# Kernel optimization log

Measured on AMD Instinct MI355X. Metric: run time of the kernel, lower is better.

## Reference

```python
import jax, jax.numpy as jnp
import numpy as np

EPS = float(jnp.finfo(jnp.float32).eps)  # torch F.rms_norm default eps


def _rope(x, cos, sin):
    # x: [B,T,H,D]; cos/sin: [1,T,1,D//2]
    d = x.shape[-1] // 2
    x1, x2 = x[..., :d], x[..., d:]
    return jnp.concatenate([x1 * cos + x2 * sin, -x1 * sin + x2 * cos], axis=-1)


def _rmsnorm(x):
    ms = jnp.mean(jnp.square(x), axis=-1, keepdims=True)
    return x * jax.lax.rsqrt(ms + EPS)


def setup_inputs() -> dict:
    key = jax.random.key(0)
    ks = jax.random.split(key, 7)
    B, T, C, H, D = 2, 2048, 2048, 16, 128
    x = jax.random.normal(ks[0], (B, T, C), dtype=jnp.float32)
    # RoPE tables (use actual rotary angles for realism)
    pos = jnp.arange(T, dtype=jnp.float32)[:, None]
    inv_freq = 1.0 / (10000.0 ** (jnp.arange(0, D // 2, dtype=jnp.float32) / (D // 2)))
    ang = pos * inv_freq[None, :]  # [T, D/2]
    cos = jnp.cos(ang)[None, :, None, :]
    sin = jnp.sin(ang)[None, :, None, :]
    w_scale = 0.02
    wq = jax.random.normal(ks[1], (C, C), dtype=jnp.float32) * w_scale
    wk = jax.random.normal(ks[2], (C, C), dtype=jnp.float32) * w_scale
    wv = jax.random.normal(ks[3], (C, C), dtype=jnp.float32) * w_scale
    wproj = jax.random.normal(ks[4], (C, C), dtype=jnp.float32) * w_scale
    return {"x": x, "cos": cos, "sin": sin, "wq": wq, "wk": wk, "wv": wv, "wproj": wproj}


def reference(x, cos, sin, wq, wk, wv, wproj):
    B, T, C = x.shape
    H, D = 16, C // 16
    q = (x @ wq.T).reshape(B, T, H, D)
    k = (x @ wk.T).reshape(B, T, H, D)
    v = (x @ wv.T).reshape(B, T, H, D)
    q = _rmsnorm(_rope(q, cos, sin))
    k = _rmsnorm(_rope(k, cos, sin))
    scale = 1.0 / jnp.sqrt(jnp.asarray(D, dtype=x.dtype))
    # causal attention: logits [B,H,T,T]
    logits = jnp.einsum('bqhd,bkhd->bhqk', q, k) * scale
    causal = jnp.tril(jnp.ones((T, T), dtype=bool))
    logits = jnp.where(causal[None, None], logits, jnp.finfo(x.dtype).min)
    attn = jax.nn.softmax(logits, axis=-1)
    y = jnp.einsum('bhqk,bkhd->bqhd', attn, v).reshape(B, T, C)
    return y @ wproj.T
```

## Files before the change

### kernel.cpp

```cpp
#include <hip/hip_runtime.h>
#include <hip/hip_bf16.h>
#include <cstdint>
#include <cstddef>

typedef unsigned short u16;
typedef unsigned int u32;
typedef __attribute__((ext_vector_type(4))) float f32x4;
typedef __attribute__((ext_vector_type(8))) __bf16 bf16x8;

#define EPS_F 1.1920928955078125e-07f
#define INV_SQRT_D 0.08838834764831845f

__device__ __forceinline__ u16 f2bf(float f) {
  union { float f; u32 u; } v; v.f = f;
  u32 r = v.u + 0x7fffu + ((v.u >> 16) & 1u);
  return (u16)(r >> 16);
}

__device__ __forceinline__ ushort4 pack_bf4(float a, float b, float c, float d) {
  ushort4 o; o.x = f2bf(a); o.y = f2bf(b); o.z = f2bf(c); o.w = f2bf(d); return o;
}

__device__ __forceinline__ void gload_lds16(const void* g, void* l) {
  __builtin_amdgcn_global_load_lds((const __attribute__((address_space(1))) u32*)g,
                                   (__attribute__((address_space(3))) u32*)l, 16, 0, 0);
}

__global__ __launch_bounds__(256) void k_cast_bf16(const float* __restrict__ src,
                                                   u16* __restrict__ dst, int n) {
  int i = (blockIdx.x * 256 + threadIdx.x) * 4;
  if (i + 3 < n) {
    float4 v = *(const float4*)(src + i);
    *(ushort4*)(dst + i) = pack_bf4(v.x, v.y, v.z, v.w);
  }
}

__global__ __launch_bounds__(256) void k_gemm_bt(const u16* __restrict__ A,
                                                 const u16* __restrict__ Bw,
                                                 float* __restrict__ C,
                                                 int M, int N, int K) {
  __shared__ __align__(16) u16 As[128 * 32];
  __shared__ __align__(16) u16 Bs[128 * 32];
  const int tid = threadIdx.x;
  const int lane = tid & 63;
  const int wid = tid >> 6;
  const int wm = wid >> 1, wn = wid & 1;
  const int l15 = lane & 15, l4 = lane >> 4;

  f32x4 acc[4][4];
#pragma unroll
  for (int i = 0; i < 4; ++i)
#pragma unroll
    for (int j = 0; j < 4; ++j) acc[i][j] = {0.f, 0.f, 0.f, 0.f};

  const u16* Ab = A + (size_t)blockIdx.x * 128 * K;
  const u16* Bb = Bw + (size_t)blockIdx.y * 128 * K;
  const int lrow = lane >> 2;
  const int scol = ((lane & 3) ^ ((lane >> 3) & 3)) * 8;
  const int rswz = (l15 >> 1) & 3;

  for (int k0 = 0; k0 < K; k0 += 32) {
    __syncthreads();
#pragma unroll
    for (int p = 0; p < 2; ++p) {
      const int chunk = wid * 2 + p;
      const int row = chunk * 16 + lrow;
      gload_lds16(Ab + (size_t)row * K + k0 + scol, &As[chunk * 512]);
      gload_lds16(Bb + (size_t)row * K + k0 + scol, &Bs[chunk * 512]);
    }
    __syncthreads();
    bf16x8 af[4], bfv[4];
#pragma unroll
    for (int i = 0; i < 4; ++i) {
      const int cb = (l4 ^ rswz) * 8;
      af[i]  = *(const bf16x8*)&As[(wm * 64 + i * 16 + l15) * 32 + cb];
      bfv[i] = *(const bf16x8*)&Bs[(wn * 64 + i * 16 + l15) * 32 + cb];
    }
#pragma unroll
    for (int i = 0; i < 4; ++i)
#pragma unroll
      for (int j = 0; j < 4; ++j)
        acc[i][j] = __builtin_amdgcn_mfma_f32_16x16x32_bf16(af[i], bfv[j], acc[i][j], 0, 0, 0);
  }

  const int r0 = blockIdx.x * 128 + wm * 64 + l4 * 4;
  const int c0 = blockIdx.y * 128 + wn * 64 + l15;
#pragma unroll
  for (int i = 0; i < 4; ++i)
#pragma unroll
    for (int j = 0; j < 4; ++j) {
      float* Cp = C + (size_t)(r0 + i * 16) * N + c0 + j * 16;
#pragma unroll
      for (int r = 0; r < 4; ++r) Cp[(size_t)r * N] = acc[i][j][r];
    }
}

__global__ __launch_bounds__(256) void k_rope_rms(const float* __restrict__ qkv,
                                                  const float* __restrict__ cosp,
                                                  const float* __restrict__ sinp,
                                                  u16* __restrict__ qb, u16* __restrict__ kb,
                                                  u16* __restrict__ vb) {
  const int T = 2048;
  const int m = blockIdx.x;
  const int b = m >> 11;
  const int t = m & 2047;
  const int tid = threadIdx.x;
  const int h = tid >> 4;
  const int d0 = (tid & 15) * 4;
  const size_t ro = (size_t)m * 6144 + h * 128;

  float4 q1 = *(const float4*)(qkv + ro + d0);
  float4 q2 = *(const float4*)(qkv + ro + d0 + 64);
  float4 k1 = *(const float4*)(qkv + ro + 2048 + d0);
  float4 k2 = *(const float4*)(qkv + ro + 2048 + d0 + 64);
  float4 v1 = *(const float4*)(qkv + ro + 4096 + d0);
  float4 v2 = *(const float4*)(qkv + ro + 4096 + d0 + 64);
  float4 cs = *(const float4*)(cosp + (size_t)t * 64 + d0);
  float4 sn = *(const float4*)(sinp + (size_t)t * 64 + d0);

  float sq = q1.x*q1.x + q1.y*q1.y + q1.z*q1.z + q1.w*q1.w
           + q2.x*q2.x + q2.y*q2.y + q2.z*q2.z + q2.w*q2.w;
  float sk = k1.x*k1.x + k1.y*k1.y + k1.z*k1.z + k1.w*k1.w
           + k2.x*k2.x + k2.y*k2.y + k2.z*k2.z + k2.w*k2.w;
#pragma unroll
  for (int o = 1; o < 16; o <<= 1) {
    sq += __shfl_xor(sq, o, 64);
    sk += __shfl_xor(sk, o, 64);
  }
  const float rq = rsqrtf(sq * (1.f / 128.f) + EPS_F) * INV_SQRT_D;
  const float rk = rsqrtf(sk * (1.f / 128.f) + EPS_F);

  const size_t ob = ((size_t)(b * 16 + h) * T + t) * 128 + d0;
  *(ushort4*)(qb + ob) = pack_bf4((q1.x*cs.x + q2.x*sn.x) * rq, (q1.y*cs.y + q2.y*sn.y) * rq,
                                  (q1.z*cs.z + q2.z*sn.z) * rq, (q1.w*cs.w + q2.w*sn.w) * rq);
  *(ushort4*)(qb + ob + 64) = pack_bf4((q2.x*cs.x - q1.x*sn.x) * rq, (q2.y*cs.y - q1.y*sn.y) * rq,
                                       (q2.z*cs.z - q1.z*sn.z) * rq, (q2.w*cs.w - q1.w*sn.w) * rq);
  *(ushort4*)(kb + ob) = pack_bf4((k1.x*cs.x + k2.x*sn.x) * rk, (k1.y*cs.y + k2.y*sn.y) * rk,
                                  (k1.z*cs.z + k2.z*sn.z) * rk, (k1.w*cs.w + k2.w*sn.w) * rk);
  *(ushort4*)(kb + ob + 64) = pack_bf4((k2.x*cs.x - k1.x*sn.x) * rk, (k2.y*cs.y - k1.y*sn.y) * rk,
                                       (k2.z*cs.z - k1.z*sn.z) * rk, (k2.w*cs.w - k1.w*sn.w) * rk);
  *(ushort4*)(vb + ob) = pack_bf4(v1.x, v1.y, v1.z, v1.w);
  *(ushort4*)(vb + ob + 64) = pack_bf4(v2.x, v2.y, v2.z, v2.w);
}

__global__ __launch_bounds__(256) void k_transpose_v(const u16* __restrict__ vb,
                                                     u16* __restrict__ vt) {
  const int T = 2048;
  __shared__ u16 tile[32][33];
  const int bh = blockIdx.z;
  const int t0 = blockIdx.x * 32;
  const int d0 = blockIdx.y * 32;
  const int tx = threadIdx.x & 31;
  const int ty = threadIdx.x >> 5;
  const size_t base = (size_t)bh * T * 128;
#pragma unroll
  for (int i = 0; i < 4; ++i)
    tile[ty + i * 8][tx] = vb[base + (size_t)(t0 + ty + i * 8) * 128 + d0 + tx];
  __syncthreads();
#pragma unroll
  for (int i = 0; i < 4; ++i)
    vt[base + (size_t)(d0 + ty + i * 8) * T + t0 + tx] = tile[tx][ty + i * 8];
}

__global__ __launch_bounds__(256) void k_attn(const u16* __restrict__ qb,
                                              const u16* __restrict__ kb,
                                              const u16* __restrict__ vt,
                                              u16* __restrict__ y) {
  const int T = 2048;
  __shared__ __align__(16) u16 Ks[64 * 128];
  __shared__ __align__(16) u16 Vs[128 * 64];
  __shared__ __align__(16) u16 Ps[64 * 72];

  const int tid = threadIdx.x;
  const int lane = tid & 63;
  const int wid = tid >> 6;
  const int bh = blockIdx.y;
  const int q0 = blockIdx.x * 64;
  const int b = bh >> 4, h = bh & 15;
  const size_t hb = (size_t)bh * T * 128;
  const int l15 = lane & 15, l4 = lane >> 4;

  bf16x8 qf[4];
  {
    const int qrow = q0 + wid * 16 + l15;
#pragma unroll
    for (int ki = 0; ki < 4; ++ki)
      qf[ki] = *(const bf16x8*)(qb + hb + (size_t)qrow * 128 + ki * 32 + l4 * 8);
  }

  float mrow[4], lsum[4];
  f32x4 oacc[8];
#pragma unroll
  for (int r = 0; r < 4; ++r) { mrow[r] = -INFINITY; lsum[r] = 0.f; }
#pragma unroll
  for (int d = 0; d < 8; ++d) oacc[d] = {0.f, 0.f, 0.f, 0.f};

  const int niter = blockIdx.x + 1;
  for (int it = 0; it < niter; ++it) {
    const int kv0 = it * 64;
    __syncthreads();
#pragma unroll
    for (int p = 0; p < 4; ++p) {
      const int chunk = wid * 4 + p;
      {
        const int row = chunk * 4 + l4;
        const int scb = l15 ^ (row & 7);
        gload_lds16(kb + hb + (size_t)(kv0 + row) * 128 + scb * 8, &Ks[chunk * 512]);
      }
      {
        const int row = chunk * 8 + (lane >> 3);
        const int scb = (lane & 7) ^ (row & 7);
        gload_lds16(vt + hb + (size_t)row * T + kv0 + scb * 8, &Vs[chunk * 512]);
      }
    }
    __syncthreads();

    f32x4 s[4];
#pragma unroll
    for (int ni = 0; ni < 4; ++ni) {
      s[ni] = {0.f, 0.f, 0.f, 0.f};
      const int r = ni * 16 + l15;
#pragma unroll
      for (int ki = 0; ki < 4; ++ki) {
        const int cb = (ki * 4 + l4) ^ (r & 7);
        bf16x8 kf = *(const bf16x8*)&Ks[r * 128 + cb * 8];
        s[ni] = __builtin_amdgcn_mfma_f32_16x16x32_bf16(qf[ki], kf, s[ni], 0, 0, 0);
      }
    }

    if (kv0 == q0) {
      const int grow = q0 + wid * 16 + l4 * 4;
      const int gcol = kv0 + l15;
#pragma unroll
      for (int ni = 0; ni < 4; ++ni)
#pragma unroll
        for (int r = 0; r < 4; ++r)
          if (gcol + ni * 16 > grow + r) s[ni][r] = -INFINITY;
    }

    float pv[4][4];
    float alpha[4];
#pragma unroll
    for (int r = 0; r < 4; ++r) {
      float mx = fmaxf(fmaxf(s[0][r], s[1][r]), fmaxf(s[2][r], s[3][r]));
#pragma unroll
      for (int o = 1; o < 16; o <<= 1) mx = fmaxf(mx, __shfl_xor(mx, o, 64));
      const float mnew = fmaxf(mrow[r], mx);
      alpha[r] = __expf(mrow[r] - mnew);
      mrow[r] = mnew;
      float ps = 0.f;
#pragma unroll
      for (int ni = 0; ni < 4; ++ni) {
        const float p = __expf(s[ni][r] - mnew);
        pv[ni][r] = p;
        ps += p;
      }
#pragma unroll
      for (int o = 1; o < 16; o <<= 1) ps += __shfl_xor(ps, o, 64);
      lsum[r] = lsum[r] * alpha[r] + ps;
    }
#pragma unroll
    for (int d = 0; d < 8; ++d) {
      f32x4 tv = oacc[d];
      tv[0] *= alpha[0]; tv[1] *= alpha[1]; tv[2] *= alpha[2]; tv[3] *= alpha[3];
      oacc[d] = tv;
    }
#pragma unroll
    for (int ni = 0; ni < 4; ++ni)
#pragma unroll
      for (int r = 0; r < 4; ++r)
        Ps[(wid * 16 + l4 * 4 + r) * 72 + ni * 16 + l15] = f2bf(pv[ni][r]);
    __syncthreads();

#pragma unroll
    for (int k2 = 0; k2 < 2; ++k2) {
      bf16x8 pa = *(const bf16x8*)&Ps[(wid * 16 + l15) * 72 + k2 * 32 + l4 * 8];
#pragma unroll
      for (int dt = 0; dt < 8; ++dt) {
        const int r = dt * 16 + l15;
        const int cb = (k2 * 4 + l4) ^ (r & 7);
        bf16x8 vf = *(const bf16x8*)&Vs[r * 64 + cb * 8];
        oacc[dt] = __builtin_amdgcn_mfma_f32_16x16x32_bf16(pa, vf, oacc[dt], 0, 0, 0);
      }
    }
  }

#pragma unroll
  for (int r = 0; r < 4; ++r) {
    const float inv = 1.f / lsum[r];
    const size_t yo = ((size_t)(b * T) + q0 + wid * 16 + l4 * 4 + r) * 2048 + h * 128;
#pragma unroll
    for (int dt = 0; dt < 8; ++dt)
      y[yo + dt * 16 + l15] = f2bf(oacc[dt][r] * inv);
  }
}

extern "C" void kernel_launch(void* const* d_in, const int* in_sizes, int n_in,
                              void* d_out, int out_size, void* d_ws, size_t ws_size,
                              hipStream_t stream) {
  const float* x     = (const float*)d_in[0];
  const float* cosp  = (const float*)d_in[1];
  const float* sinp  = (const float*)d_in[2];
  const float* wq    = (const float*)d_in[3];
  const float* wk    = (const float*)d_in[4];
  const float* wv    = (const float*)d_in[5];
  const float* wproj = (const float*)d_in[6];
  float* out = (float*)d_out;

  const int T = 2048, C = 2048;
  const int M = 2 * T;
  const int N1 = 3 * C;

  char* ws = (char*)d_ws;
  size_t off = 0;
  auto take = [&](size_t bytes) -> char* {
    char* p = ws + off;
    off += (bytes + 255) & ~(size_t)255;
    return p;
  };
  u16* xb    = (u16*)take((size_t)M * C * 2);
  u16* wqkvb = (u16*)take((size_t)N1 * C * 2);
  u16* wpb   = (u16*)take((size_t)C * C * 2);
  float* qkv = (float*)take((size_t)M * N1 * 4);
  u16* qb    = (u16*)take((size_t)M * C * 2);
  u16* kb    = (u16*)take((size_t)M * C * 2);
  u16* vb    = (u16*)take((size_t)M * C * 2);
  u16* vt    = (u16*)take((size_t)M * C * 2);
  u16* yb    = (u16*)take((size_t)M * C * 2);
  (void)ws_size; (void)in_sizes; (void)n_in; (void)out_size;

  const int nx = M * C;
  const int nw = C * C;
  k_cast_bf16<<<nx / 1024, 256, 0, stream>>>(x, xb, nx);
  k_cast_bf16<<<nw / 1024, 256, 0, stream>>>(wq, wqkvb, nw);
  k_cast_bf16<<<nw / 1024, 256, 0, stream>>>(wk, wqkvb + (size_t)C * C, nw);
  k_cast_bf16<<<nw / 1024, 256, 0, stream>>>(wv, wqkvb + (size_t)2 * C * C, nw);
  k_cast_bf16<<<nw / 1024, 256, 0, stream>>>(wproj, wpb, nw);

  k_gemm_bt<<<dim3(M / 128, N1 / 128), 256, 0, stream>>>(xb, wqkvb, qkv, M, N1, C);
  k_rope_rms<<<M, 256, 0, stream>>>(qkv, cosp, sinp, qb, kb, vb);
  k_transpose_v<<<dim3(T / 32, 128 / 32, 32), 256, 0, stream>>>(vb, vt);
  k_attn<<<dim3(T / 64, 32), 256, 0, stream>>>(qb, kb, vt, yb);
  k_gemm_bt<<<dim3(M / 128, C / 128), 256, 0, stream>>>(yb, wpb, out, M, C, C);
}
```

Measured before the change: 547.3 us.

## Double-buffer K/V tiles, pair causal query tiles, use exp2 softmax

The attention kernel now double-buffers the K and V tiles in LDS. The next tile's global-to-LDS load is issued before computing on the current one, with a single barrier per iteration instead of two. Each block processes two query tiles (qt and 31-qt), so every block gets the same amount of causal work; the grid is halved to match. The softmax scale is folded together with log2(e) into the q normalization so exp2f replaces __expf. In exchange, LDS use doubles, which may lower occupancy, and there are fewer blocks in flight.

```diff
diff --git a/kernel.cpp b/kernel.cpp
--- a/kernel.cpp
+++ b/kernel.cpp
@@ -10,6 +10,7 @@
 
 #define EPS_F 1.1920928955078125e-07f
 #define INV_SQRT_D 0.08838834764831845f
+#define LOG2E 1.4426950408889634f
 
 __device__ __forceinline__ u16 f2bf(float f) {
   union { float f; u32 u; } v; v.f = f;
@@ -127,7 +128,7 @@
     sq += __shfl_xor(sq, o, 64);
     sk += __shfl_xor(sk, o, 64);
   }
-  const float rq = rsqrtf(sq * (1.f / 128.f) + EPS_F) * INV_SQRT_D;
+  const float rq = rsqrtf(sq * (1.f / 128.f) + EPS_F) * (INV_SQRT_D * LOG2E);
   const float rk = rsqrtf(sk * (1.f / 128.f) + EPS_F);
 
   const size_t ob = ((size_t)(b * 16 + h) * T + t) * 128 + d0;
@@ -167,131 +168,148 @@
                                               const u16* __restrict__ vt,
                                               u16* __restrict__ y) {
   const int T = 2048;
-  __shared__ __align__(16) u16 Ks[64 * 128];
-  __shared__ __align__(16) u16 Vs[128 * 64];
+  __shared__ __align__(16) u16 Ks[2][64 * 128];
+  __shared__ __align__(16) u16 Vs[2][128 * 64];
   __shared__ __align__(16) u16 Ps[64 * 72];
 
   const int tid = threadIdx.x;
   const int lane = tid & 63;
   const int wid = tid >> 6;
   const int bh = blockIdx.y;
-  const int q0 = blockIdx.x * 64;
   const int b = bh >> 4, h = bh & 15;
   const size_t hb = (size_t)bh * T * 128;
   const int l15 = lane & 15, l4 = lane >> 4;
 
-  bf16x8 qf[4];
-  {
-    const int qrow = q0 + wid * 16 + l15;
-#pragma unroll
-    for (int ki = 0; ki < 4; ++ki)
-      qf[ki] = *(const bf16x8*)(qb + hb + (size_t)qrow * 128 + ki * 32 + l4 * 8);
-  }
-
-  float mrow[4], lsum[4];
-  f32x4 oacc[8];
-#pragma unroll
-  for (int r = 0; r < 4; ++r) { mrow[r] = -INFINITY; lsum[r] = 0.f; }
-#pragma unroll
-  for (int d = 0; d < 8; ++d) oacc[d] = {0.f, 0.f, 0.f, 0.f};
-
-  const int niter = blockIdx.x + 1;
-  for (int it = 0; it < niter; ++it) {
-    const int kv0 = it * 64;
-    __syncthreads();
+  auto stage = [&](int it, int buf) {
 #pragma unroll
     for (int p = 0; p < 4; ++p) {
       const int chunk = wid * 4 + p;
       {
         const int row = chunk * 4 + l4;
         const int scb = l15 ^ (row & 7);
-        gload_lds16(kb + hb + (size_t)(kv0 + row) * 128 + scb * 8, &Ks[chunk * 512]);
+        gload_lds16(kb + hb + (size_t)(it * 64 + row) * 128 + scb * 8, &Ks[buf][chunk * 512]);
       }
       {
         const int row = chunk * 8 + (lane >> 3);
         const int scb = (lane & 7) ^ (row & 7);
-        gload_lds16(vt + hb + (size_t)row * T + kv0 + scb * 8, &Vs[chunk * 512]);
-      }
-    }
-    __syncthreads();
-
-    f32x4 s[4];
-#pragma unroll
-    for (int ni = 0; ni < 4; ++ni) {
-      s[ni] = {0.f, 0.f, 0.f, 0.f};
-      const int r = ni * 16 + l15;
-#pragma unroll
-      for (int ki = 0; ki < 4; ++ki) {
-        const int cb = (ki * 4 + l4) ^ (r & 7);
-        bf16x8 kf = *(const bf16x8*)&Ks[r * 128 + cb * 8];
-        s[ni] = __builtin_amdgcn_mfma_f32_16x16x32_bf16(qf[ki], kf, s[ni], 0, 0, 0);
-      }
-    }
-
-    if (kv0 == q0) {
-      const int grow = q0 + wid * 16 + l4 * 4;
-      const int gcol = kv0 + l15;
+        gload_lds16(vt + hb + (size_t)row * T + it * 64 + scb * 8, &Vs[buf][chunk * 512]);
+      }
+    }
+  };
+
+#pragma unroll 1
+  for (int ph = 0; ph < 2; ++ph) {
+    const int qt = (ph == 0) ? (int)blockIdx.x : 31 - (int)blockIdx.x;
+    const int q0 = qt * 64;
+    const int niter = qt + 1;
+
+    bf16x8 qf[4];
+    {
+      const int qrow = q0 + wid * 16 + l15;
+#pragma unroll
+      for (int ki = 0; ki < 4; ++ki)
+        qf[ki] = *(const bf16x8*)(qb + hb + (size_t)qrow * 128 + ki * 32 + l4 * 8);
+    }
+
+    float mrow[4], lsum[4];
+    f32x4 oacc[8];
+#pragma unroll
+    for (int r = 0; r < 4; ++r) { mrow[r] = -INFINITY; lsum[r] = 0.f; }
+#pragma unroll
+    for (int d = 0; d < 8; ++d) oacc[d] = {0.f, 0.f, 0.f, 0.f};
+
+    stage(0, 0);
+    asm volatile("s_waitcnt vmcnt(0)" ::: "memory");
+    __builtin_amdgcn_s_barrier();
+    __builtin_amdgcn_sched_barrier(0);
+
+    int cur = 0;
+#pragma unroll 1
+    for (int it = 0; it < niter; ++it) {
+      if (it + 1 < niter) stage(it + 1, cur ^ 1);
+
+      f32x4 s[4];
+#pragma unroll
+      for (int ni = 0; ni < 4; ++ni) {
+        s[ni] = {0.f, 0.f, 0.f, 0.f};
+        const int r = ni * 16 + l15;
+#pragma unroll
+        for (int ki = 0; ki < 4; ++ki) {
+          const int cb = (ki * 4 + l4) ^ (r & 7);
+          bf16x8 kf = *(const bf16x8*)&Ks[cur][r * 128 + cb * 8];
+          s[ni] = __builtin_amdgcn_mfma_f32_16x16x32_bf16(qf[ki], kf, s[ni], 0, 0, 0);
+        }
+      }
+
+      if (it == niter - 1) {
+        const int grow = q0 + wid * 16 + l4 * 4;
+        const int gcol = it * 64 + l15;
+#pragma unroll
+        for (int ni = 0; ni < 4; ++ni)
+#pragma unroll
+          for (int r = 0; r < 4; ++r)
+            if (gcol + ni * 16 > grow + r) s[ni][r] = -INFINITY;
+      }
+
+      float pv[4][4];
+      float alpha[4];
+#pragma unroll
+      for (int r = 0; r < 4; ++r) {
+        float mx = fmaxf(fmaxf(s[0][r], s[1][r]), fmaxf(s[2][r], s[3][r]));
+#pragma unroll
+        for (int o = 1; o < 16; o <<= 1) mx = fmaxf(mx, __shfl_xor(mx, o, 64));
+        const float mnew = fmaxf(mrow[r], mx);
+        alpha[r] = exp2f(mrow[r] - mnew);
+        mrow[r] = mnew;
+        float ps = 0.f;
+#pragma unroll
+        for (int ni = 0; ni < 4; ++ni) {
+          const float p = exp2f(s[ni][r] - mnew);
+          pv[ni][r] = p;
+          ps += p;
+        }
+#pragma unroll
+        for (int o = 1; o < 16; o <<= 1) ps += __shfl_xor(ps, o, 64);
+        lsum[r] = lsum[r] * alpha[r] + ps;
+      }
+#pragma unroll
+      for (int d = 0; d < 8; ++d) {
+        f32x4 tv = oacc[d];
+        tv[0] *= alpha[0]; tv[1] *= alpha[1]; tv[2] *= alpha[2]; tv[3] *= alpha[3];
+        oacc[d] = tv;
+      }
 #pragma unroll
       for (int ni = 0; ni < 4; ++ni)
 #pragma unroll
         for (int r = 0; r < 4; ++r)
-          if (gcol + ni * 16 > grow + r) s[ni][r] = -INFINITY;
-    }
-
-    float pv[4][4];
-    float alpha[4];
+          Ps[(wid * 16 + l4 * 4 + r) * 72 + ni * 16 + l15] = f2bf(pv[ni][r]);
+
+#pragma unroll
+      for (int k2 = 0; k2 < 2; ++k2) {
+        bf16x8 pa = *(const bf16x8*)&Ps[(wid * 16 + l15) * 72 + k2 * 32 + l4 * 8];
+#pragma unroll
+        for (int dt = 0; dt < 8; ++dt) {
+          const int r = dt * 16 + l15;
+          const int cb = (k2 * 4 + l4) ^ (r & 7);
+          bf16x8 vf = *(const bf16x8*)&Vs[cur][r * 64 + cb * 8];
+          oacc[dt] = __builtin_amdgcn_mfma_f32_16x16x32_bf16(pa, vf, oacc[dt], 0, 0, 0);
+        }
+      }
+
+      asm volatile("s_waitcnt vmcnt(0)" ::: "memory");
+      __builtin_amdgcn_s_barrier();
+      __builtin_amdgcn_sched_barrier(0);
+      cur ^= 1;
+    }
+
 #pragma unroll
     for (int r = 0; r < 4; ++r) {
-      float mx = fmaxf(fmaxf(s[0][r], s[1][r]), fmaxf(s[2][r], s[3][r]));
-#pragma unroll
-      for (int o = 1; o < 16; o <<= 1) mx = fmaxf(mx, __shfl_xor(mx, o, 64));
-      const float mnew = fmaxf(mrow[r], mx);
-      alpha[r] = __expf(mrow[r] - mnew);
-      mrow[r] = mnew;
-      float ps = 0.f;
-#pragma unroll
-      for (int ni = 0; ni < 4; ++ni) {
-        const float p = __expf(s[ni][r] - mnew);
-        pv[ni][r] = p;
-        ps += p;
-      }
-#pragma unroll
-      for (int o = 1; o < 16; o <<= 1) ps += __shfl_xor(ps, o, 64);
-      lsum[r] = lsum[r] * alpha[r] + ps;
-    }
-#pragma unroll
-    for (int d = 0; d < 8; ++d) {
-      f32x4 tv = oacc[d];
-      tv[0] *= alpha[0]; tv[1] *= alpha[1]; tv[2] *= alpha[2]; tv[3] *= alpha[3];
-      oacc[d] = tv;
-    }
-#pragma unroll
-    for (int ni = 0; ni < 4; ++ni)
-#pragma unroll
-      for (int r = 0; r < 4; ++r)
-        Ps[(wid * 16 + l4 * 4 + r) * 72 + ni * 16 + l15] = f2bf(pv[ni][r]);
-    __syncthreads();
-
-#pragma unroll
-    for (int k2 = 0; k2 < 2; ++k2) {
-      bf16x8 pa = *(const bf16x8*)&Ps[(wid * 16 + l15) * 72 + k2 * 32 + l4 * 8];
-#pragma unroll
-      for (int dt = 0; dt < 8; ++dt) {
-        const int r = dt * 16 + l15;
-        const int cb = (k2 * 4 + l4) ^ (r & 7);
-        bf16x8 vf = *(const bf16x8*)&Vs[r * 64 + cb * 8];
-        oacc[dt] = __builtin_amdgcn_mfma_f32_16x16x32_bf16(pa, vf, oacc[dt], 0, 0, 0);
-      }
-    }
-  }
-
-#pragma unroll
-  for (int r = 0; r < 4; ++r) {
-    const float inv = 1.f / lsum[r];
-    const size_t yo = ((size_t)(b * T) + q0 + wid * 16 + l4 * 4 + r) * 2048 + h * 128;
-#pragma unroll
-    for (int dt = 0; dt < 8; ++dt)
-      y[yo + dt * 16 + l15] = f2bf(oacc[dt][r] * inv);
+      const float inv = 1.f / lsum[r];
+      const size_t yo = ((size_t)(b * T) + q0 + wid * 16 + l4 * 4 + r) * 2048 + h * 128;
+#pragma unroll
+      for (int dt = 0; dt < 8; ++dt)
+        y[yo + dt * 16 + l15] = f2bf(oacc[dt][r] * inv);
+    }
   }
 }
 
@@ -340,6 +358,6 @@
   k_gemm_bt<<<dim3(M / 128, N1 / 128), 256, 0, stream>>>(xb, wqkvb, qkv, M, N1, C);
   k_rope_rms<<<M, 256, 0, stream>>>(qkv, cosp, sinp, qb, kb, vb);
   k_transpose_v<<<dim3(T / 32, 128 / 32, 32), 256, 0, stream>>>(vb, vt);
-  k_attn<<<dim3(T / 64, 32), 256, 0, stream>>>(qb, kb, vt, yb);
+  k_attn<<<dim3(16, 32), 256, 0, stream>>>(qb, kb, vt, yb);
   k_gemm_bt<<<dim3(M / 128, C / 128), 256, 0, stream>>>(yb, wpb, out, M, C, C);
 }
```

After: 472.7 us. 1.16x faster.
